# Kernel optimization log

Hardware: AMD Instinct MI355X
Metric: run time of the kernel (lower is better)

The kernel has to match this reference:

```python
import jax, jax.numpy as jnp
import numpy as np

N_NODES = 50000
N_EDGES = 600000
IN_CH = 128
HID_CH = 128
OUT_CH = 64
NUM_GRAPHS = 512


def _gcn_conv(x, W, b, src, dst, n):
    # PyG GCNConv (eval): h = D^{-1/2} (A + I) D^{-1/2} (x W) + b
    h = x @ W  # [N, C]
    loop = jnp.arange(n)
    s = jnp.concatenate([src, loop])  # add self-loops
    d = jnp.concatenate([dst, loop])
    deg = jax.ops.segment_sum(jnp.ones_like(d, dtype=h.dtype), d, num_segments=n)
    dinv = jnp.where(deg > 0, jax.lax.rsqrt(deg), 0.0)
    coef = dinv[s] * dinv[d]  # [E+N]
    msg = h[s] * coef[:, None]  # gather + scale
    out = jax.ops.segment_sum(msg, d, num_segments=n)  # scatter-add
    return out + b


def setup_inputs() -> dict:
    key = jax.random.key(0)
    ks = jax.random.split(key, 10)
    x = jax.random.normal(ks[0], (N_NODES, IN_CH), dtype=jnp.float32)
    edge_index = jax.random.randint(ks[1], (2, N_EDGES), 0, N_NODES, dtype=jnp.int64)
    batch = jnp.sort(jax.random.randint(ks[2], (N_NODES,), 0, NUM_GRAPHS, dtype=jnp.int64))
    sc1 = 1.0 / np.sqrt(IN_CH)
    sc2 = 1.0 / np.sqrt(HID_CH)
    W1 = jax.random.uniform(ks[3], (IN_CH, HID_CH), jnp.float32, -sc1, sc1)
    b1 = jnp.zeros((HID_CH,), jnp.float32)
    W2 = jax.random.uniform(ks[4], (HID_CH, HID_CH), jnp.float32, -sc2, sc2)
    b2 = jnp.zeros((HID_CH,), jnp.float32)
    Wlin = jax.random.uniform(ks[5], (HID_CH, OUT_CH), jnp.float32, -sc2, sc2)
    blin = jax.random.uniform(ks[6], (OUT_CH,), jnp.float32, -sc2, sc2)
    return {"x": x, "W1": W1, "b1": b1, "W2": W2, "b2": b2,
            "Wlin": Wlin, "blin": blin, "edge_index": edge_index, "batch": batch}


def reference(x, W1, b1, W2, b2, Wlin, blin, edge_index, batch):
    n = x.shape[0]
    src, dst = edge_index[0], edge_index[1]
    h = jax.nn.relu(_gcn_conv(x, W1, b1, src, dst, n))
    # dropout: identity in eval mode (training=False)
    h = jax.nn.relu(_gcn_conv(h, W2, b2, src, dst, n))
    # global mean pool over graphs
    summed = jax.ops.segment_sum(h, batch, num_segments=NUM_GRAPHS)
    cnt = jax.ops.segment_sum(jnp.ones((n,), h.dtype), batch, num_segments=NUM_GRAPHS)
    pooled = summed / jnp.maximum(cnt, 1.0)[:, None]
    return pooled @ Wlin + blin  # [NUM_GRAPHS, OUT_CH]
```

## Files before the change

kernel.cpp:

```cpp
#include <hip/hip_runtime.h>

#define N_NODES 50000
#define N_EDGES 600000
#define CH 128
#define NUM_GRAPHS 512
#define OUT_CH 64
#define DSH 6
#define DSTRIDE 64
#define BSHIFT 9
#define NBUCK 98
#define BCAP 8192
#define L1_EPT 16
#define L1_EDGES (256 * L1_EPT)
#define L1_BLOCKS ((N_EDGES + L1_EDGES - 1) / L1_EDGES)

typedef unsigned int uint32;
typedef __attribute__((ext_vector_type(8))) short short8;
typedef __attribute__((ext_vector_type(4))) float floatx4;

__device__ __forceinline__ uint32 bfpack(float a, float b) {
    uint32 ua = __builtin_bit_cast(uint32, a);
    uint32 ub = __builtin_bit_cast(uint32, b);
    ua = (ua + 0x7fffu + ((ua >> 16) & 1u)) >> 16;
    ub = (ub + 0x7fffu + ((ub >> 16) & 1u)) >> 16;
    return (ub << 16) | ua;
}
__device__ __forceinline__ unsigned short bfr(float f) {
    uint32 u = __builtin_bit_cast(uint32, f);
    u = (u + 0x7fffu + ((u >> 16) & 1u)) >> 16;
    return (unsigned short)u;
}
__device__ __forceinline__ float bf_lo(uint32 v) {
    return __builtin_bit_cast(float, v << 16);
}
__device__ __forceinline__ float bf_hi(uint32 v) {
    return __builtin_bit_cast(float, v & 0xffff0000u);
}

__global__ void k_prep(const float* __restrict__ W1, const float* __restrict__ W2,
                       unsigned short* __restrict__ W1t, unsigned short* __restrict__ W2t,
                       int* __restrict__ gcnt) {
    int idx = blockIdx.x * 256 + threadIdx.x;
    if (idx < NBUCK) gcnt[idx] = 0;
    if (idx < 32768) {
        int mat = idx >> 14;
        int rem = idx & 16383;
        int k = rem >> 7, c = rem & 127;
        const float* W = mat ? W2 : W1;
        unsigned short* Wt = mat ? W2t : W1t;
        Wt[c * 128 + k] = bfr(W[k * 128 + c]);
    }
}

__global__ __launch_bounds__(256) void k_bin(const int* __restrict__ src,
                                             const int* __restrict__ dst,
                                             int* __restrict__ gcnt,
                                             uint2* __restrict__ binned) {
    __shared__ int hist[NBUCK];
    __shared__ int lstart[NBUCK];
    __shared__ int base[NBUCK];
    __shared__ int curs[NBUCK];
    __shared__ int scan[128];
    __shared__ uint2 stage[L1_EDGES];
    int tid = threadIdx.x;
    if (tid < NBUCK) { hist[tid] = 0; curs[tid] = 0; }
    __syncthreads();

    int blk0 = blockIdx.x * L1_EDGES;
    int ss[L1_EPT], dd[L1_EPT];
    #pragma unroll
    for (int i = 0; i < L1_EPT; ++i) {
        int e = blk0 + i * 256 + tid;
        if (e < N_EDGES) {
            ss[i] = src[e];
            dd[i] = dst[e];
            atomicAdd(&hist[dd[i] >> BSHIFT], 1);
        } else {
            dd[i] = -1;
        }
    }
    __syncthreads();
    if (tid < 128) scan[tid] = (tid < NBUCK) ? hist[tid] : 0;
    __syncthreads();
    #pragma unroll
    for (int st = 1; st < 128; st <<= 1) {
        int t = 0;
        if (tid < 128 && tid >= st) t = scan[tid - st];
        __syncthreads();
        if (tid < 128) scan[tid] += t;
        __syncthreads();
    }
    if (tid < NBUCK) {
        lstart[tid] = scan[tid] - hist[tid];
        base[tid] = atomicAdd(&gcnt[tid], hist[tid]);
    }
    __syncthreads();
    #pragma unroll
    for (int i = 0; i < L1_EPT; ++i) {
        if (dd[i] >= 0) {
            int b = dd[i] >> BSHIFT;
            int loc = lstart[b] + atomicAdd(&curs[b], 1);
            stage[loc] = make_uint2((uint32)ss[i], (uint32)dd[i]);
        }
    }
    __syncthreads();
    int total = min(N_EDGES - blk0, L1_EDGES);
    for (int i = tid; i < total; i += 256) {
        uint2 e = stage[i];
        int b = (int)(e.y >> BSHIFT);
        int slot = base[b] + (i - lstart[b]);
        if (slot < BCAP) binned[(size_t)b * BCAP + slot] = e;
    }
}

__global__ __launch_bounds__(256) void k_build(const uint2* __restrict__ binned,
                                               const int* __restrict__ gcnt,
                                               int* __restrict__ cur,
                                               int* __restrict__ srcs) {
    __shared__ int cl[1 << BSHIFT];
    int b = blockIdx.x;
    int tid = threadIdx.x;
    #pragma unroll
    for (int i = tid; i < (1 << BSHIFT); i += 256) cl[i] = 0;
    __syncthreads();
    int n = min(gcnt[b], BCAP);
    int nb = b << BSHIFT;
    for (int i = tid; i < n; i += 256) {
        uint2 e = binned[(size_t)b * BCAP + i];
        int d = (int)e.y;
        int p = atomicAdd(&cl[d - nb], 1);
        if (p < DSTRIDE) srcs[(d << DSH) + p] = (int)e.x;
    }
    __syncthreads();
    #pragma unroll
    for (int i = tid; i < (1 << BSHIFT); i += 256) {
        int d = nb + i;
        if (d < N_NODES) cur[d] = cl[i];
    }
}

template <bool AF32>
__global__ __launch_bounds__(256, 2) void k_gemm(const void* __restrict__ Av,
                                                 const unsigned short* __restrict__ Wt,
                                                 const int* __restrict__ cur,
                                                 unsigned short* __restrict__ outb) {
    __shared__ __align__(16) unsigned short as_[128][136];
    __shared__ __align__(16) unsigned short bs[128][136];
    int tid = threadIdx.x;
    int row0 = blockIdx.x * 128;

    #pragma unroll
    for (int it = 0; it < 8; ++it) {
        int idx = it * 256 + tid;
        int r = idx >> 4, seg = idx & 15;
        int gr = min(row0 + r, N_NODES - 1);
        if (AF32) {
            const float4* ap = (const float4*)((const float*)Av + (size_t)gr * 128 + seg * 8);
            float4 v0 = ap[0], v1 = ap[1];
            uint4 pk;
            pk.x = bfpack(v0.x, v0.y); pk.y = bfpack(v0.z, v0.w);
            pk.z = bfpack(v1.x, v1.y); pk.w = bfpack(v1.z, v1.w);
            *(uint4*)&as_[r][seg * 8] = pk;
        } else {
            *(uint4*)&as_[r][seg * 8] =
                *(const uint4*)((const unsigned short*)Av + (size_t)gr * 128 + seg * 8);
        }
    }
    #pragma unroll
    for (int it = 0; it < 8; ++it) {
        int idx = it * 256 + tid;
        int c = idx >> 4, seg = idx & 15;
        *(uint4*)&bs[c][seg * 8] = *(const uint4*)&Wt[c * 128 + seg * 8];
    }
    __syncthreads();

    int w = tid >> 6, lane = tid & 63, q = lane >> 4, m = lane & 15;
    int q8 = q * 8;
    floatx4 acc[2][8];
    #pragma unroll
    for (int rt = 0; rt < 2; ++rt)
        #pragma unroll
        for (int ct = 0; ct < 8; ++ct) {
            floatx4 z = {0.f, 0.f, 0.f, 0.f};
            acc[rt][ct] = z;
        }

    #pragma unroll
    for (int kc = 0; kc < 128; kc += 32) {
        short8 a0 = *(const short8*)&as_[w * 32 + m][kc + q8];
        short8 a1 = *(const short8*)&as_[w * 32 + 16 + m][kc + q8];
        #pragma unroll
        for (int ct = 0; ct < 8; ++ct) {
            short8 b = *(const short8*)&bs[ct * 16 + m][kc + q8];
            acc[0][ct] = __builtin_amdgcn_mfma_f32_16x16x32_bf16(a0, b, acc[0][ct], 0, 0, 0);
            acc[1][ct] = __builtin_amdgcn_mfma_f32_16x16x32_bf16(a1, b, acc[1][ct], 0, 0, 0);
        }
    }

    #pragma unroll
    for (int rt = 0; rt < 2; ++rt) {
        #pragma unroll
        for (int i = 0; i < 4; ++i) {
            int gr = row0 + w * 32 + rt * 16 + q * 4 + i;
            if (gr < N_NODES) {
                float sc = rsqrtf((float)(cur[gr] + 1));
                #pragma unroll
                for (int ct = 0; ct < 8; ++ct) {
                    outb[(size_t)gr * 128 + ct * 16 + m] = bfr(acc[rt][ct][i] * sc);
                }
            }
        }
    }
}

template <bool BF16OUT>
__global__ __launch_bounds__(256) void k_agg(const uint32* __restrict__ hb,
                                             const int* __restrict__ cnt_arr,
                                             const int* __restrict__ srcs,
                                             const float* __restrict__ bias,
                                             void* __restrict__ outv) {
    int node = __builtin_amdgcn_readfirstlane(blockIdx.x * 4 + (threadIdx.x >> 6));
    int lane = threadIdx.x & 63;

    int cnt = cnt_arr[node];
    float dn = rsqrtf((float)(cnt + 1));
    uint32 vs = hb[node * 64 + lane];
    float ax = bf_lo(vs), ay = bf_hi(vs);

    int start = node << DSH;
    int last = start + cnt - 1;
    for (int j = 0; j < cnt; j += 8) {
        int i0 = start + j;
        int i1 = min(i0 + 1, last);
        int i2 = min(i0 + 2, last);
        int i3 = min(i0 + 3, last);
        int i4 = min(i0 + 4, last);
        int i5 = min(i0 + 5, last);
        int i6 = min(i0 + 6, last);
        int i7 = min(i0 + 7, last);
        int s0 = srcs[i0], s1 = srcs[i1], s2 = srcs[i2], s3 = srcs[i3];
        int s4 = srcs[i4], s5 = srcs[i5], s6 = srcs[i6], s7 = srcs[i7];
        uint32 v0 = hb[s0 * 64 + lane];
        uint32 v1 = hb[s1 * 64 + lane];
        uint32 v2 = hb[s2 * 64 + lane];
        uint32 v3 = hb[s3 * 64 + lane];
        uint32 v4 = hb[s4 * 64 + lane];
        uint32 v5 = hb[s5 * 64 + lane];
        uint32 v6 = hb[s6 * 64 + lane];
        uint32 v7 = hb[s7 * 64 + lane];
        int rem = cnt - j;
        v1 = (rem > 1) ? v1 : 0u;
        v2 = (rem > 2) ? v2 : 0u;
        v3 = (rem > 3) ? v3 : 0u;
        v4 = (rem > 4) ? v4 : 0u;
        v5 = (rem > 5) ? v5 : 0u;
        v6 = (rem > 6) ? v6 : 0u;
        v7 = (rem > 7) ? v7 : 0u;
        ax += bf_lo(v0); ay += bf_hi(v0);
        ax += bf_lo(v1); ay += bf_hi(v1);
        ax += bf_lo(v2); ay += bf_hi(v2);
        ax += bf_lo(v3); ay += bf_hi(v3);
        ax += bf_lo(v4); ay += bf_hi(v4);
        ax += bf_lo(v5); ay += bf_hi(v5);
        ax += bf_lo(v6); ay += bf_hi(v6);
        ax += bf_lo(v7); ay += bf_hi(v7);
    }
    float2 b = ((const float2*)bias)[lane];
    ax = fmaxf(ax * dn + b.x, 0.f);
    ay = fmaxf(ay * dn + b.y, 0.f);
    if (BF16OUT) ((uint32*)outv)[node * 64 + lane] = bfpack(ax, ay);
    else         ((float2*)outv)[node * 64 + lane] = make_float2(ax, ay);
}

__global__ __launch_bounds__(256) void k_pool_linear(const float* __restrict__ h,
                                                     const int* __restrict__ batch,
                                                     const float* __restrict__ Wl,
                                                     const float* __restrict__ bl,
                                                     float* __restrict__ out) {
    __shared__ int sb[2];
    __shared__ float4 sacc[256];
    __shared__ float xr[CH];
    __shared__ float po[4][OUT_CH];
    int g = blockIdx.x;
    int tid = threadIdx.x;
    if (tid < 2) {
        int target = g + tid;
        int lo = 0, hi = N_NODES;
        while (lo < hi) {
            int mid = (lo + hi) >> 1;
            if (batch[mid] < target) lo = mid + 1; else hi = mid;
        }
        sb[tid] = lo;
    }
    __syncthreads();
    int lo = sb[0], hi = sb[1];
    int q = tid & 31;
    int r = tid >> 5;
    const float4* h4 = (const float4*)h;
    float4 acc = make_float4(0.f, 0.f, 0.f, 0.f);
    for (int i = lo + r; i < hi; i += 8) {
        float4 v = h4[(size_t)i * 32 + q];
        acc.x += v.x; acc.y += v.y; acc.z += v.z; acc.w += v.w;
    }
    sacc[tid] = acc;
    __syncthreads();
    if (r == 0) {
        #pragma unroll
        for (int p = 1; p < 8; ++p) {
            float4 t = sacc[q + p * 32];
            acc.x += t.x; acc.y += t.y; acc.z += t.z; acc.w += t.w;
        }
        float inv = 1.f / (float)((hi - lo) > 0 ? (hi - lo) : 1);
        xr[q * 4 + 0] = acc.x * inv;
        xr[q * 4 + 1] = acc.y * inv;
        xr[q * 4 + 2] = acc.z * inv;
        xr[q * 4 + 3] = acc.w * inv;
    }
    __syncthreads();
    int c = tid & 63;
    int kh = tid >> 6;
    float o = 0.f;
    #pragma unroll 8
    for (int k = kh * 32; k < kh * 32 + 32; ++k) o += xr[k] * Wl[k * OUT_CH + c];
    po[kh][c] = o;
    __syncthreads();
    if (tid < OUT_CH) {
        float v = bl[tid] + po[0][tid] + po[1][tid] + po[2][tid] + po[3][tid];
        out[g * OUT_CH + tid] = v;
    }
}

extern "C" void kernel_launch(void* const* d_in, const int* in_sizes, int n_in,
                              void* d_out, int out_size, void* d_ws, size_t ws_size,
                              hipStream_t stream) {
    const float* x    = (const float*)d_in[0];
    const float* W1   = (const float*)d_in[1];
    const float* b1   = (const float*)d_in[2];
    const float* W2   = (const float*)d_in[3];
    const float* b2   = (const float*)d_in[4];
    const float* Wlin = (const float*)d_in[5];
    const float* blin = (const float*)d_in[6];
    const int* ei     = (const int*)d_in[7];
    const int* batch  = (const int*)d_in[8];
    const int* esrc = ei;
    const int* edst = ei + N_EDGES;
    float* out = (float*)d_out;

    char* w = (char*)d_ws;
    size_t o = 0;
    float* hA            = (float*)(w + o);          o += (size_t)N_NODES * CH * 4;
    unsigned short* hb   = (unsigned short*)(w + o); o += (size_t)N_NODES * CH * 2;
    uint32* habf         = (uint32*)(w + o);         o += (size_t)N_NODES * 64 * 4;
    unsigned short* W1t  = (unsigned short*)(w + o); o += 16384 * 2;
    unsigned short* W2t  = (unsigned short*)(w + o); o += 16384 * 2;
    int* srcs            = (int*)(w + o);            o += (size_t)N_NODES * DSTRIDE * 4;
    int* cur             = (int*)(w + o);            o += 200704;
    uint2* binned        = (uint2*)(w + o);          o += (size_t)NBUCK * BCAP * 8;
    int* gcnt            = (int*)(w + o);            o += 512;
    (void)ws_size; (void)in_sizes; (void)n_in; (void)out_size;

    dim3 b256(256);
    k_prep<<<dim3(196), b256, 0, stream>>>(W1, W2, W1t, W2t, gcnt);
    k_bin<<<dim3(L1_BLOCKS), b256, 0, stream>>>(esrc, edst, gcnt, binned);
    k_build<<<dim3(NBUCK), b256, 0, stream>>>(binned, gcnt, cur, srcs);

    dim3 gG((N_NODES + 127) / 128);
    dim3 gA(N_NODES / 4);
    k_gemm<true><<<gG, b256, 0, stream>>>(x, W1t, cur, hb);
    k_agg<true><<<gA, b256, 0, stream>>>((const uint32*)hb, cur, srcs, b1, habf);
    k_gemm<false><<<gG, b256, 0, stream>>>(habf, W2t, cur, hb);
    k_agg<false><<<gA, b256, 0, stream>>>((const uint32*)hb, cur, srcs, b2, hA);
    k_pool_linear<<<dim3(NUM_GRAPHS), b256, 0, stream>>>(hA, batch, Wlin, blin, out);
}
```

Measured before the change: 192.6 us.

## Split GEMM output into channel-quarter tables and aggregate per quarter

The GEMM now writes its bf16 output as four column-quarter tables (32 channels each, node-major within a quarter). The aggregation kernel launches a second grid dimension over quarters. Each wavefront handles one node-quarter, with four 16-lane groups gathering different neighbors in parallel, and the partial sums are reduced with cross-lane shuffles. The goal is smaller per-table working sets for better cache locality and more edges in flight per wavefront. The cost is four times as many blocks, repeated index loads and degree reads, and shuffle reductions.

```diff
diff --git a/kernel.cpp b/kernel.cpp
--- a/kernel.cpp
+++ b/kernel.cpp
@@ -206,7 +206,8 @@
                 float sc = rsqrtf((float)(cur[gr] + 1));
                 #pragma unroll
                 for (int ct = 0; ct < 8; ++ct) {
-                    outb[(size_t)gr * 128 + ct * 16 + m] = bfr(acc[rt][ct][i] * sc);
+                    outb[((size_t)(ct >> 1) * N_NODES + gr) * 32 + (ct & 1) * 16 + m] =
+                        bfr(acc[rt][ct][i] * sc);
                 }
             }
         }
@@ -214,62 +215,49 @@
 }
 
 template <bool BF16OUT>
-__global__ __launch_bounds__(256) void k_agg(const uint32* __restrict__ hb,
-                                             const int* __restrict__ cnt_arr,
-                                             const int* __restrict__ srcs,
-                                             const float* __restrict__ bias,
-                                             void* __restrict__ outv) {
+__global__ __launch_bounds__(256) void k_agg4(const uint32* __restrict__ hbq,
+                                              const int* __restrict__ cnt_arr,
+                                              const int* __restrict__ srcs,
+                                              const float* __restrict__ bias,
+                                              void* __restrict__ outv) {
     int node = __builtin_amdgcn_readfirstlane(blockIdx.x * 4 + (threadIdx.x >> 6));
+    int q    = __builtin_amdgcn_readfirstlane(blockIdx.y);
     int lane = threadIdx.x & 63;
+    int grp = lane >> 4;
+    int c   = lane & 15;
 
     int cnt = cnt_arr[node];
     float dn = rsqrtf((float)(cnt + 1));
-    uint32 vs = hb[node * 64 + lane];
-    float ax = bf_lo(vs), ay = bf_hi(vs);
-
+    const uint32* tab = hbq + (size_t)q * N_NODES * 16;
+
+    float ax = 0.f, ay = 0.f;
     int start = node << DSH;
-    int last = start + cnt - 1;
+    int cl = cnt - 1;
     for (int j = 0; j < cnt; j += 8) {
-        int i0 = start + j;
-        int i1 = min(i0 + 1, last);
-        int i2 = min(i0 + 2, last);
-        int i3 = min(i0 + 3, last);
-        int i4 = min(i0 + 4, last);
-        int i5 = min(i0 + 5, last);
-        int i6 = min(i0 + 6, last);
-        int i7 = min(i0 + 7, last);
-        int s0 = srcs[i0], s1 = srcs[i1], s2 = srcs[i2], s3 = srcs[i3];
-        int s4 = srcs[i4], s5 = srcs[i5], s6 = srcs[i6], s7 = srcs[i7];
-        uint32 v0 = hb[s0 * 64 + lane];
-        uint32 v1 = hb[s1 * 64 + lane];
-        uint32 v2 = hb[s2 * 64 + lane];
-        uint32 v3 = hb[s3 * 64 + lane];
-        uint32 v4 = hb[s4 * 64 + lane];
-        uint32 v5 = hb[s5 * 64 + lane];
-        uint32 v6 = hb[s6 * 64 + lane];
-        uint32 v7 = hb[s7 * 64 + lane];
-        int rem = cnt - j;
-        v1 = (rem > 1) ? v1 : 0u;
-        v2 = (rem > 2) ? v2 : 0u;
-        v3 = (rem > 3) ? v3 : 0u;
-        v4 = (rem > 4) ? v4 : 0u;
-        v5 = (rem > 5) ? v5 : 0u;
-        v6 = (rem > 6) ? v6 : 0u;
-        v7 = (rem > 7) ? v7 : 0u;
-        ax += bf_lo(v0); ay += bf_hi(v0);
-        ax += bf_lo(v1); ay += bf_hi(v1);
-        ax += bf_lo(v2); ay += bf_hi(v2);
-        ax += bf_lo(v3); ay += bf_hi(v3);
-        ax += bf_lo(v4); ay += bf_hi(v4);
-        ax += bf_lo(v5); ay += bf_hi(v5);
-        ax += bf_lo(v6); ay += bf_hi(v6);
-        ax += bf_lo(v7); ay += bf_hi(v7);
-    }
-    float2 b = ((const float2*)bias)[lane];
+        int pa = j + grp;
+        int pb = pa + 4;
+        int sa = srcs[start + min(pa, cl)];
+        int sb = srcs[start + min(pb, cl)];
+        uint32 va = tab[(size_t)sa * 16 + c];
+        uint32 vb = tab[(size_t)sb * 16 + c];
+        va = (pa < cnt) ? va : 0u;
+        vb = (pb < cnt) ? vb : 0u;
+        ax += bf_lo(va); ay += bf_hi(va);
+        ax += bf_lo(vb); ay += bf_hi(vb);
+    }
+    ax += __shfl_xor(ax, 16, 64); ax += __shfl_xor(ax, 32, 64);
+    ay += __shfl_xor(ay, 16, 64); ay += __shfl_xor(ay, 32, 64);
+
+    uint32 vs = tab[(size_t)node * 16 + c];
+    ax += bf_lo(vs); ay += bf_hi(vs);
+
+    float2 b = ((const float2*)bias)[q * 16 + c];
     ax = fmaxf(ax * dn + b.x, 0.f);
     ay = fmaxf(ay * dn + b.y, 0.f);
-    if (BF16OUT) ((uint32*)outv)[node * 64 + lane] = bfpack(ax, ay);
-    else         ((float2*)outv)[node * 64 + lane] = make_float2(ax, ay);
+    if (grp == 0) {
+        if (BF16OUT) ((uint32*)outv)[(size_t)node * 64 + q * 16 + c] = bfpack(ax, ay);
+        else ((float2*)outv)[(size_t)node * 64 + q * 16 + c] = make_float2(ax, ay);
+    }
 }
 
 __global__ __launch_bounds__(256) void k_pool_linear(const float* __restrict__ h,
@@ -349,7 +337,7 @@
     char* w = (char*)d_ws;
     size_t o = 0;
     float* hA            = (float*)(w + o);          o += (size_t)N_NODES * CH * 4;
-    unsigned short* hb   = (unsigned short*)(w + o); o += (size_t)N_NODES * CH * 2;
+    uint32* hbq          = (uint32*)(w + o);         o += (size_t)N_NODES * CH * 2;
     uint32* habf         = (uint32*)(w + o);         o += (size_t)N_NODES * 64 * 4;
     unsigned short* W1t  = (unsigned short*)(w + o); o += 16384 * 2;
     unsigned short* W2t  = (unsigned short*)(w + o); o += 16384 * 2;
@@ -365,10 +353,10 @@
     k_build<<<dim3(NBUCK), b256, 0, stream>>>(binned, gcnt, cur, srcs);
 
     dim3 gG((N_NODES + 127) / 128);
-    dim3 gA(N_NODES / 4);
-    k_gemm<true><<<gG, b256, 0, stream>>>(x, W1t, cur, hb);
-    k_agg<true><<<gA, b256, 0, stream>>>((const uint32*)hb, cur, srcs, b1, habf);
-    k_gemm<false><<<gG, b256, 0, stream>>>(habf, W2t, cur, hb);
-    k_agg<false><<<gA, b256, 0, stream>>>((const uint32*)hb, cur, srcs, b2, hA);
+    dim3 gA4(N_NODES / 4, 4);
+    k_gemm<true><<<gG, b256, 0, stream>>>(x, W1t, cur, (unsigned short*)hbq);
+    k_agg4<true><<<gA4, b256, 0, stream>>>(hbq, cur, srcs, b1, habf);
+    k_gemm<false><<<gG, b256, 0, stream>>>(habf, W2t, cur, (unsigned short*)hbq);
+    k_agg4<false><<<gA4, b256, 0, stream>>>(hbq, cur, srcs, b2, hA);
     k_pool_linear<<<dim3(NUM_GRAPHS), b256, 0, stream>>>(hA, batch, Wlin, blin, out);
 }
```

After: 265.4 us. 37.8% more time.

## Partition neighbour lists by source slice and aggregate in phased passes

Applied to the files above, without the earlier changes.

k_build now counts each destination's incoming edges per source quarter (four slices of 12500 nodes) and stores them sorted by slice, with packed per-slice counts in cnt4. The aggregation kernel is restructured as a persistent grid of 2048 blocks. Each wave handles 7 nodes and sweeps the four source slices in order, so that concurrently executing waves gather from a narrower region of the feature table and get better L2/cache locality. This costs a second pass over the binned edges in k_build and more registers in the aggregation kernel. The phases are not synchronised across waves, so the locality benefit depends on waves staying roughly in step.

```diff
diff --git a/kernel.cpp b/kernel.cpp
--- a/kernel.cpp
+++ b/kernel.cpp
@@ -13,6 +13,9 @@
 #define L1_EPT 16
 #define L1_EDGES (256 * L1_EPT)
 #define L1_BLOCKS ((N_EDGES + L1_EDGES - 1) / L1_EDGES)
+#define SLICE_N 12500
+#define AGG_BLOCKS 2048
+#define NPW 7
 
 typedef unsigned int uint32;
 typedef __attribute__((ext_vector_type(8))) short short8;
@@ -35,6 +38,10 @@
 }
 __device__ __forceinline__ float bf_hi(uint32 v) {
     return __builtin_bit_cast(float, v & 0xffff0000u);
+}
+__device__ __forceinline__ int slice_of(int s) {
+    return (s >= 2 * SLICE_N) ? ((s >= 3 * SLICE_N) ? 3 : 2)
+                              : ((s >= SLICE_N) ? 1 : 0);
 }
 
 __global__ void k_prep(const float* __restrict__ W1, const float* __restrict__ W2,
@@ -116,26 +123,37 @@
 __global__ __launch_bounds__(256) void k_build(const uint2* __restrict__ binned,
                                                const int* __restrict__ gcnt,
                                                int* __restrict__ cur,
+                                               uint32* __restrict__ cnt4,
                                                int* __restrict__ srcs) {
-    __shared__ int cl[1 << BSHIFT];
+    __shared__ int c4[1 << BSHIFT][4];
     int b = blockIdx.x;
     int tid = threadIdx.x;
-    #pragma unroll
-    for (int i = tid; i < (1 << BSHIFT); i += 256) cl[i] = 0;
+    for (int i = tid; i < (1 << BSHIFT); i += 256) {
+        c4[i][0] = 0; c4[i][1] = 0; c4[i][2] = 0; c4[i][3] = 0;
+    }
     __syncthreads();
     int n = min(gcnt[b], BCAP);
     int nb = b << BSHIFT;
     for (int i = tid; i < n; i += 256) {
         uint2 e = binned[(size_t)b * BCAP + i];
-        int d = (int)e.y;
-        int p = atomicAdd(&cl[d - nb], 1);
-        if (p < DSTRIDE) srcs[(d << DSH) + p] = (int)e.x;
-    }
-    __syncthreads();
-    #pragma unroll
+        atomicAdd(&c4[(int)e.y - nb][slice_of((int)e.x)], 1);
+    }
+    __syncthreads();
     for (int i = tid; i < (1 << BSHIFT); i += 256) {
         int d = nb + i;
-        if (d < N_NODES) cur[d] = cl[i];
+        if (d < N_NODES) {
+            int c0 = c4[i][0], c1 = c4[i][1], c2 = c4[i][2], c3 = c4[i][3];
+            cur[d] = c0 + c1 + c2 + c3;
+            cnt4[d] = (uint32)c0 | ((uint32)c1 << 8) | ((uint32)c2 << 16) | ((uint32)c3 << 24);
+            c4[i][0] = 0; c4[i][1] = c0; c4[i][2] = c0 + c1; c4[i][3] = c0 + c1 + c2;
+        }
+    }
+    __syncthreads();
+    for (int i = tid; i < n; i += 256) {
+        uint2 e = binned[(size_t)b * BCAP + i];
+        int s = (int)e.x, d = (int)e.y;
+        int p = atomicAdd(&c4[d - nb][slice_of(s)], 1);
+        if (p < DSTRIDE) srcs[(d << DSH) + p] = s;
     }
 }
 
@@ -214,62 +232,88 @@
 }
 
 template <bool BF16OUT>
-__global__ __launch_bounds__(256) void k_agg(const uint32* __restrict__ hb,
-                                             const int* __restrict__ cnt_arr,
-                                             const int* __restrict__ srcs,
-                                             const float* __restrict__ bias,
-                                             void* __restrict__ outv) {
-    int node = __builtin_amdgcn_readfirstlane(blockIdx.x * 4 + (threadIdx.x >> 6));
+__global__ __launch_bounds__(256, 8) void k_agg_ph(const uint32* __restrict__ hb,
+                                                   const uint32* __restrict__ cnt4,
+                                                   const int* __restrict__ srcs,
+                                                   const float* __restrict__ bias,
+                                                   void* __restrict__ outv) {
+    int wid = __builtin_amdgcn_readfirstlane(blockIdx.x * 4 + (threadIdx.x >> 6));
     int lane = threadIdx.x & 63;
 
-    int cnt = cnt_arr[node];
-    float dn = rsqrtf((float)(cnt + 1));
-    uint32 vs = hb[node * 64 + lane];
-    float ax = bf_lo(vs), ay = bf_hi(vs);
-
-    int start = node << DSH;
-    int last = start + cnt - 1;
-    for (int j = 0; j < cnt; j += 8) {
-        int i0 = start + j;
-        int i1 = min(i0 + 1, last);
-        int i2 = min(i0 + 2, last);
-        int i3 = min(i0 + 3, last);
-        int i4 = min(i0 + 4, last);
-        int i5 = min(i0 + 5, last);
-        int i6 = min(i0 + 6, last);
-        int i7 = min(i0 + 7, last);
-        int s0 = srcs[i0], s1 = srcs[i1], s2 = srcs[i2], s3 = srcs[i3];
-        int s4 = srcs[i4], s5 = srcs[i5], s6 = srcs[i6], s7 = srcs[i7];
-        uint32 v0 = hb[s0 * 64 + lane];
-        uint32 v1 = hb[s1 * 64 + lane];
-        uint32 v2 = hb[s2 * 64 + lane];
-        uint32 v3 = hb[s3 * 64 + lane];
-        uint32 v4 = hb[s4 * 64 + lane];
-        uint32 v5 = hb[s5 * 64 + lane];
-        uint32 v6 = hb[s6 * 64 + lane];
-        uint32 v7 = hb[s7 * 64 + lane];
-        int rem = cnt - j;
-        v1 = (rem > 1) ? v1 : 0u;
-        v2 = (rem > 2) ? v2 : 0u;
-        v3 = (rem > 3) ? v3 : 0u;
-        v4 = (rem > 4) ? v4 : 0u;
-        v5 = (rem > 5) ? v5 : 0u;
-        v6 = (rem > 6) ? v6 : 0u;
-        v7 = (rem > 7) ? v7 : 0u;
-        ax += bf_lo(v0); ay += bf_hi(v0);
-        ax += bf_lo(v1); ay += bf_hi(v1);
-        ax += bf_lo(v2); ay += bf_hi(v2);
-        ax += bf_lo(v3); ay += bf_hi(v3);
-        ax += bf_lo(v4); ay += bf_hi(v4);
-        ax += bf_lo(v5); ay += bf_hi(v5);
-        ax += bf_lo(v6); ay += bf_hi(v6);
-        ax += bf_lo(v7); ay += bf_hi(v7);
-    }
-    float2 b = ((const float2*)bias)[lane];
-    ax = fmaxf(ax * dn + b.x, 0.f);
-    ay = fmaxf(ay * dn + b.y, 0.f);
-    if (BF16OUT) ((uint32*)outv)[node * 64 + lane] = bfpack(ax, ay);
-    else         ((float2*)outv)[node * 64 + lane] = make_float2(ax, ay);
+    float ax[NPW], ay[NPW];
+    #pragma unroll
+    for (int k = 0; k < NPW; ++k) { ax[k] = 0.f; ay[k] = 0.f; }
+
+    for (int p = 0; p < 4; ++p) {
+        int lo = p * SLICE_N;
+        #pragma unroll
+        for (int k = 0; k < NPW; ++k) {
+            int node = wid + k * (AGG_BLOCKS * 4);
+            if (node >= N_NODES) continue;
+            uint32 u = cnt4[node];
+            int c0 = u & 255, c1 = (u >> 8) & 255, c2 = (u >> 16) & 255;
+            int off = ((p > 0) ? c0 : 0) + ((p > 1) ? c1 : 0) + ((p > 2) ? c2 : 0);
+            int cp = (p == 0) ? c0 : (p == 1) ? c1 : (p == 2) ? c2 : (int)(u >> 24);
+            float a_x = ax[k], a_y = ay[k];
+            int base = (node << DSH) + off;
+            int last = base + cp - 1;
+            for (int j = 0; j < cp; j += 8) {
+                int i0 = base + j;
+                int i1 = min(i0 + 1, last);
+                int i2 = min(i0 + 2, last);
+                int i3 = min(i0 + 3, last);
+                int i4 = min(i0 + 4, last);
+                int i5 = min(i0 + 5, last);
+                int i6 = min(i0 + 6, last);
+                int i7 = min(i0 + 7, last);
+                int s0 = srcs[i0], s1 = srcs[i1], s2 = srcs[i2], s3 = srcs[i3];
+                int s4 = srcs[i4], s5 = srcs[i5], s6 = srcs[i6], s7 = srcs[i7];
+                uint32 v0 = hb[s0 * 64 + lane];
+                uint32 v1 = hb[s1 * 64 + lane];
+                uint32 v2 = hb[s2 * 64 + lane];
+                uint32 v3 = hb[s3 * 64 + lane];
+                uint32 v4 = hb[s4 * 64 + lane];
+                uint32 v5 = hb[s5 * 64 + lane];
+                uint32 v6 = hb[s6 * 64 + lane];
+                uint32 v7 = hb[s7 * 64 + lane];
+                int rem = cp - j;
+                v1 = (rem > 1) ? v1 : 0u;
+                v2 = (rem > 2) ? v2 : 0u;
+                v3 = (rem > 3) ? v3 : 0u;
+                v4 = (rem > 4) ? v4 : 0u;
+                v5 = (rem > 5) ? v5 : 0u;
+                v6 = (rem > 6) ? v6 : 0u;
+                v7 = (rem > 7) ? v7 : 0u;
+                a_x += bf_lo(v0); a_y += bf_hi(v0);
+                a_x += bf_lo(v1); a_y += bf_hi(v1);
+                a_x += bf_lo(v2); a_y += bf_hi(v2);
+                a_x += bf_lo(v3); a_y += bf_hi(v3);
+                a_x += bf_lo(v4); a_y += bf_hi(v4);
+                a_x += bf_lo(v5); a_y += bf_hi(v5);
+                a_x += bf_lo(v6); a_y += bf_hi(v6);
+                a_x += bf_lo(v7); a_y += bf_hi(v7);
+            }
+            if ((unsigned)(node - lo) < (unsigned)SLICE_N) {
+                uint32 vs = hb[node * 64 + lane];
+                a_x += bf_lo(vs); a_y += bf_hi(vs);
+            }
+            ax[k] = a_x; ay[k] = a_y;
+        }
+    }
+
+    float2 bb = ((const float2*)bias)[lane];
+    #pragma unroll
+    for (int k = 0; k < NPW; ++k) {
+        int node = wid + k * (AGG_BLOCKS * 4);
+        if (node >= N_NODES) continue;
+        uint32 u = cnt4[node];
+        int cnt = (u & 255) + ((u >> 8) & 255) + ((u >> 16) & 255) + (int)(u >> 24);
+        float dn = rsqrtf((float)(cnt + 1));
+        float rx = fmaxf(ax[k] * dn + bb.x, 0.f);
+        float ry = fmaxf(ay[k] * dn + bb.y, 0.f);
+        if (BF16OUT) ((uint32*)outv)[node * 64 + lane] = bfpack(rx, ry);
+        else         ((float2*)outv)[node * 64 + lane] = make_float2(rx, ry);
+    }
 }
 
 __global__ __launch_bounds__(256) void k_pool_linear(const float* __restrict__ h,
@@ -355,6 +399,7 @@
     unsigned short* W2t  = (unsigned short*)(w + o); o += 16384 * 2;
     int* srcs            = (int*)(w + o);            o += (size_t)N_NODES * DSTRIDE * 4;
     int* cur             = (int*)(w + o);            o += 200704;
+    uint32* cnt4         = (uint32*)(w + o);         o += 200704;
     uint2* binned        = (uint2*)(w + o);          o += (size_t)NBUCK * BCAP * 8;
     int* gcnt            = (int*)(w + o);            o += 512;
     (void)ws_size; (void)in_sizes; (void)n_in; (void)out_size;
@@ -362,13 +407,13 @@
     dim3 b256(256);
     k_prep<<<dim3(196), b256, 0, stream>>>(W1, W2, W1t, W2t, gcnt);
     k_bin<<<dim3(L1_BLOCKS), b256, 0, stream>>>(esrc, edst, gcnt, binned);
-    k_build<<<dim3(NBUCK), b256, 0, stream>>>(binned, gcnt, cur, srcs);
+    k_build<<<dim3(NBUCK), b256, 0, stream>>>(binned, gcnt, cur, cnt4, srcs);
 
     dim3 gG((N_NODES + 127) / 128);
-    dim3 gA(N_NODES / 4);
+    dim3 gA(AGG_BLOCKS);
     k_gemm<true><<<gG, b256, 0, stream>>>(x, W1t, cur, hb);
-    k_agg<true><<<gA, b256, 0, stream>>>((const uint32*)hb, cur, srcs, b1, habf);
+    k_agg_ph<true><<<gA, b256, 0, stream>>>((const uint32*)hb, cnt4, srcs, b1, habf);
     k_gemm<false><<<gG, b256, 0, stream>>>(habf, W2t, cur, hb);
-    k_agg<false><<<gA, b256, 0, stream>>>((const uint32*)hb, cur, srcs, b2, hA);
+    k_agg_ph<false><<<gA, b256, 0, stream>>>((const uint32*)hb, cnt4, srcs, b2, hA);
     k_pool_linear<<<dim3(NUM_GRAPHS), b256, 0, stream>>>(hA, batch, Wlin, blin, out);
 }
```

Measured after the change: 283.9 us. 47.4% more time.
